# Kernel optimization log

Hardware: AMD Instinct MI355X
Metric: run time of the kernel (lower is better)

## Reference

```python
import jax, jax.numpy as jnp
import numpy as np

B, T, LAGS, H, F = 4096, 256, 32, 128, 2


def setup_inputs() -> dict:
    key = jax.random.key(0)
    ks = jax.random.split(key, 6)
    s = lambda n: 1.0 / np.sqrt(n)
    return {
        "inputs": jax.random.normal(ks[0], (B, T, F), jnp.float32),
        "Wx": jax.random.normal(ks[1], (F, H), jnp.float32) * s(F),
        "Wh": jax.random.normal(ks[2], (H, H), jnp.float32) * s(H),
        "b": jnp.zeros((H,), jnp.float32),
        "Wd": jax.random.normal(ks[3], (H, 1), jnp.float32) * s(H),
        "bd": jnp.zeros((1,), jnp.float32),
        "alpha": jax.random.uniform(ks[4], (1, 1), jnp.float32),
        "lags": LAGS,
    }


def reference(inputs, Wx, Wh, b, Wd, bd, alpha, lags):
    # alpha constrained to [0, 1] (MinMax constraint / clamp in call)
    a = jnp.clip(alpha, 0.0, 1.0)  # [1,1]
    Bsz = inputs.shape[0]
    h0 = jnp.zeros((Bsz, Wh.shape[0]), inputs.dtype)

    def cell(h, x):
        # SimpleRNN cell: tanh(x Wx + h Wh + b)
        return jnp.tanh(x @ Wx + h @ Wh + b)

    # ---- warmup: run RNN over first `lags` steps of the full 2-feature input
    warm_xs = jnp.transpose(inputs[:, :lags], (1, 0, 2))  # [lags, B, F]

    def warm_step(h, x):
        return cell(h, x), None

    h, _ = jax.lax.scan(warm_step, h0, warm_xs)
    pred = h @ Wd + bd  # [B, 1] first prediction (appended un-smoothed)

    # step n consumes exogenous inputs[:, lags + n - 1, 0]
    exog = jnp.transpose(inputs[:, lags:-1, 0])  # [T-lags-1, B]

    def ar_step(carry, e):
        h, pred, es = carry
        x = jnp.concatenate([e[:, None], pred], axis=-1)  # [B, 2]
        h = cell(h, x)
        pred = h @ Wd + bd
        es = a * pred + (1.0 - a) * es  # exponential smoothing blend
        return (h, pred, es), es

    _, es_seq = jax.lax.scan(ar_step, (h, pred, pred), exog)  # [T-lags-1, B, 1]

    preds = jnp.concatenate([pred[None], es_seq], axis=0)  # [T-lags, B, 1]
    return jnp.transpose(preds, (1, 0, 2))  # [B, T-lags, 1]
```

## Files before the change

kernel.cpp:

```cpp
#include <hip/hip_runtime.h>

namespace {

constexpr int kB = 4096;
constexpr int kT = 256;
constexpr int kLags = 32;
constexpr int kH = 128;
constexpr int kSteps = 255;
constexpr int kOut = 224;
constexpr int kMT = 16;
constexpr int kThreads = 256;
constexpr int kHS = 136;
constexpr int kOS = 225;
constexpr int kHLO = 2 * kMT * kHS;

constexpr float kZS = 2.8853900817779268f;

typedef __attribute__((ext_vector_type(8))) short short8;
typedef __attribute__((ext_vector_type(4))) float f32x4;

struct __align__(16) SMem {
    unsigned short hhi[2][kMT][kHS];
    unsigned short hlo[2][kMT][kHS];
    float x0T[kT][kMT];
    float x1wT[kLags][kMT];
    float pbuf[2][4][kMT];
    float obuf[kMT][kOS];
};

__device__ __forceinline__ unsigned short bf16_rne(float f) {
    unsigned u = __builtin_bit_cast(unsigned, f);
    u += 0x7FFFu + ((u >> 16) & 1u);
    return (unsigned short)(u >> 16);
}
__device__ __forceinline__ float bf16_f32(unsigned short h) {
    unsigned u = ((unsigned)h) << 16;
    return __builtin_bit_cast(float, u);
}
__device__ __forceinline__ float tanh_from_zs(float zs) {
    float e = __builtin_amdgcn_exp2f(zs);
    return fmaf(-2.0f, __builtin_amdgcn_rcpf(e + 1.0f), 1.0f);
}
__device__ __forceinline__ unsigned bf16_rne_hibits(float f) {
    unsigned u = __builtin_bit_cast(unsigned, f);
    return (u + (0x7FFFu + ((u >> 16) & 1u))) & 0xFFFF0000u;
}

__global__ __launch_bounds__(kThreads, 1)
void arx_rnn_es_kernel(const float* __restrict__ inputs,
                       const float* __restrict__ Wx,
                       const float* __restrict__ Wh,
                       const float* __restrict__ bias,
                       const float* __restrict__ Wd,
                       const float* __restrict__ bd,
                       const float* __restrict__ alpha,
                       float* __restrict__ out) {
    __shared__ SMem sm;
    const int tid  = threadIdx.x;
    const int b0   = blockIdx.x * kMT;
    const int lane = tid & 63;
    const int w    = tid >> 6;
    const int n    = lane & 15;
    const int q    = lane >> 4;

    for (int idx = tid; idx < kMT * kT; idx += kThreads) {
        const int mm = idx >> 8;
        const int t  = idx & 255;
        float2 v = ((const float2*)inputs)[(size_t)(b0 + mm) * kT + t];
        sm.x0T[t][mm] = v.x;
        if (t < kLags) sm.x1wT[t][mm] = v.y;
    }
    for (int idx = tid; idx < kMT * kHS; idx += kThreads) {
        ((unsigned short*)sm.hhi[0])[idx] = 0;
        ((unsigned short*)sm.hlo[0])[idx] = 0;
    }

    const float av  = fminf(fmaxf(alpha[0], 0.0f), 1.0f);
    const float bdv = bd[0];

    f32x4 sb2v[2], swx0v[2], swx1ev[2], sbpv[2];
#pragma unroll
    for (int t = 0; t < 2; ++t) {
#pragma unroll
        for (int r = 0; r < 4; ++r) {
            const int colE = w * 32 + t * 16 + q * 4 + r;
            const float bc = bias[colE];
            const float w0 = Wx[colE];
            const float w1 = Wx[kH + colE];
            sb2v[t][r]   = kZS * bc;
            swx0v[t][r]  = kZS * w0;
            swx1ev[t][r] = kZS * w1;
            sbpv[t][r]   = kZS * (bc + bdv * w1);
        }
    }
    __syncthreads();

    const f32x4 zero4 = {0.0f, 0.0f, 0.0f, 0.0f};
    int p = 0;

    {
        short8 whh[2][4], whl[2][4];
#pragma unroll
        for (int t = 0; t < 2; ++t) {
            const int colw = w * 32 + t * 16 + n;
#pragma unroll
            for (int c = 0; c < 4; ++c) {
#pragma unroll
                for (int j = 0; j < 8; ++j) {
                    const int k = c * 32 + q * 8 + j;
                    float wv = kZS * Wh[(size_t)k * kH + colw];
                    unsigned short hi = bf16_rne(wv);
                    whh[t][c][j] = (short)hi;
                    whl[t][c][j] = (short)bf16_rne(wv - bf16_f32(hi));
                }
            }
        }

#pragma unroll 1
        for (int st = 0; st < kLags; ++st) {
            const float x0s = sm.x0T[st][n];
            const float x1s = sm.x1wT[st][n];

            const unsigned short* hb = (const unsigned short*)&sm.hhi[p][n][0];
            unsigned short* hw = (unsigned short*)&sm.hhi[p ^ 1][n][0];

            short8 bh[4], bl[4];
#pragma unroll
            for (int c = 0; c < 4; ++c) {
                bh[c] = *(const short8*)(hb + c * 32 + 8 * q);
                bl[c] = *(const short8*)(hb + kHLO + c * 32 + 8 * q);
            }

            f32x4 a1[2], a2[2], a3[2];
#pragma unroll
            for (int t = 0; t < 2; ++t) {
                f32x4 xi;
#pragma unroll
                for (int r = 0; r < 4; ++r)
                    xi[r] = fmaf(x0s, swx0v[t][r], x1s * swx1ev[t][r]);
                a1[t] = __builtin_amdgcn_mfma_f32_16x16x32_bf16(whh[t][0], bh[0], sb2v[t], 0, 0, 0);
                a2[t] = __builtin_amdgcn_mfma_f32_16x16x32_bf16(whl[t][0], bh[0], zero4,   0, 0, 0);
                a3[t] = __builtin_amdgcn_mfma_f32_16x16x32_bf16(whh[t][0], bl[0], xi,      0, 0, 0);
#pragma unroll
                for (int c = 1; c < 4; ++c) {
                    a1[t] = __builtin_amdgcn_mfma_f32_16x16x32_bf16(whh[t][c], bh[c], a1[t], 0, 0, 0);
                    a2[t] = __builtin_amdgcn_mfma_f32_16x16x32_bf16(whl[t][c], bh[c], a2[t], 0, 0, 0);
                    a3[t] = __builtin_amdgcn_mfma_f32_16x16x32_bf16(whh[t][c], bl[c], a3[t], 0, 0, 0);
                }
            }

#pragma unroll
            for (int t = 0; t < 2; ++t) {
                unsigned rb[4], db[4];
#pragma unroll
                for (int r = 0; r < 4; ++r) {
                    float zs = (a1[t][r] + a2[t][r]) + a3[t][r];
                    float hf = tanh_from_zs(zs);
                    rb[r] = bf16_rne_hibits(hf);
                    float d = hf - __builtin_bit_cast(float, rb[r]);
                    db[r] = __builtin_bit_cast(unsigned, d);
                }
                uint2 uh, ul;
                uh.x = __builtin_amdgcn_perm(rb[1], rb[0], 0x07060302u);
                uh.y = __builtin_amdgcn_perm(rb[3], rb[2], 0x07060302u);
                ul.x = __builtin_amdgcn_perm(db[1], db[0], 0x07060302u);
                ul.y = __builtin_amdgcn_perm(db[3], db[2], 0x07060302u);
                *(uint2*)(hw + w * 32 + t * 16 + q * 4) = uh;
                *(uint2*)(hw + kHLO + w * 32 + t * 16 + q * 4) = ul;
            }

            __syncthreads();
            p ^= 1;
        }
    }

    short8 fhh[2][4], fhl[2][4], dhw;
    {
#pragma unroll
        for (int t = 0; t < 2; ++t) {
            const int colw = w * 32 + t * 16 + n;
            const float wx1w = Wx[kH + colw];
#pragma unroll
            for (int c = 0; c < 4; ++c) {
#pragma unroll
                for (int j = 0; j < 8; ++j) {
                    const int k = c * 32 + q * 8 + j;
                    float wv = kZS * fmaf(Wd[k], wx1w, Wh[(size_t)k * kH + colw]);
                    unsigned short hi = bf16_rne(wv);
                    fhh[t][c][j] = (short)hi;
                    fhl[t][c][j] = (short)bf16_rne(wv - bf16_f32(hi));
                }
            }
        }
#pragma unroll
        for (int j = 0; j < 8; ++j)
            dhw[j] = (short)bf16_rne(Wd[w * 32 + q * 8 + j]);
    }

    float es = 0.0f;

#pragma unroll 1
    for (int st = kLags; st < kSteps; ++st) {
        const float x0s = sm.x0T[st][n];

        const unsigned short* hb = (const unsigned short*)&sm.hhi[p][n][0];
        unsigned short* hw = (unsigned short*)&sm.hhi[p ^ 1][n][0];

        short8 bh[4], bl[4];
#pragma unroll
        for (int c = 0; c < 4; ++c) {
            bh[c] = *(const short8*)(hb + c * 32 + 8 * q);
            bl[c] = *(const short8*)(hb + kHLO + c * 32 + 8 * q);
        }
        short8 bhP = *(const short8*)(hb + w * 32 + 8 * q);

        f32x4 a1[2], a2[2], a3[2];
#pragma unroll
        for (int t = 0; t < 2; ++t) {
            f32x4 xi;
#pragma unroll
            for (int r = 0; r < 4; ++r) xi[r] = x0s * swx0v[t][r];
            a1[t] = __builtin_amdgcn_mfma_f32_16x16x32_bf16(fhh[t][0], bh[0], sbpv[t], 0, 0, 0);
            a2[t] = __builtin_amdgcn_mfma_f32_16x16x32_bf16(fhl[t][0], bh[0], zero4,   0, 0, 0);
            a3[t] = __builtin_amdgcn_mfma_f32_16x16x32_bf16(fhh[t][0], bl[0], xi,      0, 0, 0);
#pragma unroll
            for (int c = 1; c < 4; ++c) {
                a1[t] = __builtin_amdgcn_mfma_f32_16x16x32_bf16(fhh[t][c], bh[c], a1[t], 0, 0, 0);
                a2[t] = __builtin_amdgcn_mfma_f32_16x16x32_bf16(fhl[t][c], bh[c], a2[t], 0, 0, 0);
                a3[t] = __builtin_amdgcn_mfma_f32_16x16x32_bf16(fhh[t][c], bl[c], a3[t], 0, 0, 0);
            }
        }

        f32x4 P = __builtin_amdgcn_mfma_f32_16x16x32_bf16(dhw, bhP, zero4, 0, 0, 0);
        if (q == 0) sm.pbuf[p][w][n] = P[0];

        if (w == 0 && q == 0 && st > kLags) {
            float pv = ((sm.pbuf[p ^ 1][0][n] + sm.pbuf[p ^ 1][1][n]) +
                        (sm.pbuf[p ^ 1][2][n] + sm.pbuf[p ^ 1][3][n])) + bdv;
            const int m = st - kLags - 1;
            es = (m == 0) ? pv : fmaf(av, pv - es, es);
            sm.obuf[n][m] = es;
        }

#pragma unroll
        for (int t = 0; t < 2; ++t) {
            unsigned rb[4], db[4];
#pragma unroll
            for (int r = 0; r < 4; ++r) {
                float zs = (a1[t][r] + a2[t][r]) + a3[t][r];
                float hf = tanh_from_zs(zs);
                rb[r] = bf16_rne_hibits(hf);
                float d = hf - __builtin_bit_cast(float, rb[r]);
                db[r] = __builtin_bit_cast(unsigned, d);
            }
            uint2 uh, ul;
            uh.x = __builtin_amdgcn_perm(rb[1], rb[0], 0x07060302u);
            uh.y = __builtin_amdgcn_perm(rb[3], rb[2], 0x07060302u);
            ul.x = __builtin_amdgcn_perm(db[1], db[0], 0x07060302u);
            ul.y = __builtin_amdgcn_perm(db[3], db[2], 0x07060302u);
            *(uint2*)(hw + w * 32 + t * 16 + q * 4) = uh;
            *(uint2*)(hw + kHLO + w * 32 + t * 16 + q * 4) = ul;
        }

        __syncthreads();
        p ^= 1;
    }

    if (w == 0 && q == 0) {
        float pv = ((sm.pbuf[p ^ 1][0][n] + sm.pbuf[p ^ 1][1][n]) +
                    (sm.pbuf[p ^ 1][2][n] + sm.pbuf[p ^ 1][3][n])) + bdv;
        es = fmaf(av, pv - es, es);
        sm.obuf[n][kOut - 2] = es;
    }
    {
        const unsigned short* hb = (const unsigned short*)&sm.hhi[p][n][0];
        short8 bhP = *(const short8*)(hb + w * 32 + 8 * q);
        f32x4 P = __builtin_amdgcn_mfma_f32_16x16x32_bf16(dhw, bhP, zero4, 0, 0, 0);
        if (q == 0) sm.pbuf[p][w][n] = P[0];
    }
    __syncthreads();
    if (w == 0 && q == 0) {
        float pv = ((sm.pbuf[p][0][n] + sm.pbuf[p][1][n]) +
                    (sm.pbuf[p][2][n] + sm.pbuf[p][3][n])) + bdv;
        es = fmaf(av, pv - es, es);
        sm.obuf[n][kOut - 1] = es;
    }

    __syncthreads();
    for (int idx = tid; idx < kMT * kOut; idx += kThreads) {
        const int mm = idx / kOut;
        const int t  = idx - mm * kOut;
        out[(size_t)(b0 + mm) * kOut + t] = sm.obuf[mm][t];
    }
}

}

extern "C" void kernel_launch(void* const* d_in, const int* in_sizes, int n_in,
                              void* d_out, int out_size, void* d_ws, size_t ws_size,
                              hipStream_t stream) {
    const float* inputs = (const float*)d_in[0];
    const float* Wx     = (const float*)d_in[1];
    const float* Wh     = (const float*)d_in[2];
    const float* bias   = (const float*)d_in[3];
    const float* Wd     = (const float*)d_in[4];
    const float* bd     = (const float*)d_in[5];
    const float* alpha  = (const float*)d_in[6];

    arx_rnn_es_kernel<<<kB / kMT, kThreads, 0, stream>>>(
        inputs, Wx, Wh, bias, Wd, bd, alpha, (float*)d_out);
}
```

Baseline: 252.4 us.

## Split hidden columns across eight waves instead of four per block

Doubles the block to 512 threads so each of eight waves owns a 16-column tile of the hidden state rather than two 16-column tiles per wave. Each recurrent step then has a shorter serial MFMA chain per wave and more waves to hide latency. The prediction dot product stays on the first four waves. In exchange every step's barrier now spans twice as many waves, and launch bounds request two blocks per CU, which may not be reachable given the LDS footprint.

Result: faster. 216.6 us (-14.2%).

```diff
diff --git a/kernel.cpp b/kernel.cpp
--- a/kernel.cpp
+++ b/kernel.cpp
@@ -9,7 +9,7 @@
 constexpr int kSteps = 255;
 constexpr int kOut = 224;
 constexpr int kMT = 16;
-constexpr int kThreads = 256;
+constexpr int kThreads = 512;
 constexpr int kHS = 136;
 constexpr int kOS = 225;
 constexpr int kHLO = 2 * kMT * kHS;
@@ -46,7 +46,7 @@
     return (u + (0x7FFFu + ((u >> 16) & 1u))) & 0xFFFF0000u;
 }
 
-__global__ __launch_bounds__(kThreads, 1)
+__global__ __launch_bounds__(kThreads, 2)
 void arx_rnn_es_kernel(const float* __restrict__ inputs,
                        const float* __restrict__ Wx,
                        const float* __restrict__ Wh,
@@ -78,20 +78,17 @@
     const float av  = fminf(fmaxf(alpha[0], 0.0f), 1.0f);
     const float bdv = bd[0];
 
-    f32x4 sb2v[2], swx0v[2], swx1ev[2], sbpv[2];
-#pragma unroll
-    for (int t = 0; t < 2; ++t) {
-#pragma unroll
-        for (int r = 0; r < 4; ++r) {
-            const int colE = w * 32 + t * 16 + q * 4 + r;
-            const float bc = bias[colE];
-            const float w0 = Wx[colE];
-            const float w1 = Wx[kH + colE];
-            sb2v[t][r]   = kZS * bc;
-            swx0v[t][r]  = kZS * w0;
-            swx1ev[t][r] = kZS * w1;
-            sbpv[t][r]   = kZS * (bc + bdv * w1);
-        }
+    f32x4 sb2v, swx0v, swx1ev, sbpv;
+#pragma unroll
+    for (int r = 0; r < 4; ++r) {
+        const int colE = w * 16 + q * 4 + r;
+        const float bc = bias[colE];
+        const float w0 = Wx[colE];
+        const float w1 = Wx[kH + colE];
+        sb2v[r]   = kZS * bc;
+        swx0v[r]  = kZS * w0;
+        swx1ev[r] = kZS * w1;
+        sbpv[r]   = kZS * (bc + bdv * w1);
     }
     __syncthreads();
 
@@ -99,10 +96,9 @@
     int p = 0;
 
     {
-        short8 whh[2][4], whl[2][4];
-#pragma unroll
-        for (int t = 0; t < 2; ++t) {
-            const int colw = w * 32 + t * 16 + n;
+        short8 whh[4], whl[4];
+        {
+            const int colw = w * 16 + n;
 #pragma unroll
             for (int c = 0; c < 4; ++c) {
 #pragma unroll
@@ -110,8 +106,8 @@
                     const int k = c * 32 + q * 8 + j;
                     float wv = kZS * Wh[(size_t)k * kH + colw];
                     unsigned short hi = bf16_rne(wv);
-                    whh[t][c][j] = (short)hi;
-                    whl[t][c][j] = (short)bf16_rne(wv - bf16_f32(hi));
+                    whh[c][j] = (short)hi;
+                    whl[c][j] = (short)bf16_rne(wv - bf16_f32(hi));
                 }
             }
         }
@@ -131,70 +127,66 @@
                 bl[c] = *(const short8*)(hb + kHLO + c * 32 + 8 * q);
             }
 
-            f32x4 a1[2], a2[2], a3[2];
-#pragma unroll
-            for (int t = 0; t < 2; ++t) {
-                f32x4 xi;
-#pragma unroll
-                for (int r = 0; r < 4; ++r)
-                    xi[r] = fmaf(x0s, swx0v[t][r], x1s * swx1ev[t][r]);
-                a1[t] = __builtin_amdgcn_mfma_f32_16x16x32_bf16(whh[t][0], bh[0], sb2v[t], 0, 0, 0);
-                a2[t] = __builtin_amdgcn_mfma_f32_16x16x32_bf16(whl[t][0], bh[0], zero4,   0, 0, 0);
-                a3[t] = __builtin_amdgcn_mfma_f32_16x16x32_bf16(whh[t][0], bl[0], xi,      0, 0, 0);
-#pragma unroll
-                for (int c = 1; c < 4; ++c) {
-                    a1[t] = __builtin_amdgcn_mfma_f32_16x16x32_bf16(whh[t][c], bh[c], a1[t], 0, 0, 0);
-                    a2[t] = __builtin_amdgcn_mfma_f32_16x16x32_bf16(whl[t][c], bh[c], a2[t], 0, 0, 0);
-                    a3[t] = __builtin_amdgcn_mfma_f32_16x16x32_bf16(whh[t][c], bl[c], a3[t], 0, 0, 0);
-                }
-            }
-
-#pragma unroll
-            for (int t = 0; t < 2; ++t) {
-                unsigned rb[4], db[4];
-#pragma unroll
-                for (int r = 0; r < 4; ++r) {
-                    float zs = (a1[t][r] + a2[t][r]) + a3[t][r];
-                    float hf = tanh_from_zs(zs);
-                    rb[r] = bf16_rne_hibits(hf);
-                    float d = hf - __builtin_bit_cast(float, rb[r]);
-                    db[r] = __builtin_bit_cast(unsigned, d);
-                }
-                uint2 uh, ul;
-                uh.x = __builtin_amdgcn_perm(rb[1], rb[0], 0x07060302u);
-                uh.y = __builtin_amdgcn_perm(rb[3], rb[2], 0x07060302u);
-                ul.x = __builtin_amdgcn_perm(db[1], db[0], 0x07060302u);
-                ul.y = __builtin_amdgcn_perm(db[3], db[2], 0x07060302u);
-                *(uint2*)(hw + w * 32 + t * 16 + q * 4) = uh;
-                *(uint2*)(hw + kHLO + w * 32 + t * 16 + q * 4) = ul;
-            }
+            f32x4 xi;
+#pragma unroll
+            for (int r = 0; r < 4; ++r)
+                xi[r] = fmaf(x0s, swx0v[r], x1s * swx1ev[r]);
+
+            f32x4 a1 = __builtin_amdgcn_mfma_f32_16x16x32_bf16(whh[0], bh[0], sb2v, 0, 0, 0);
+            f32x4 a2 = __builtin_amdgcn_mfma_f32_16x16x32_bf16(whl[0], bh[0], zero4, 0, 0, 0);
+            f32x4 a3 = __builtin_amdgcn_mfma_f32_16x16x32_bf16(whh[0], bl[0], xi,   0, 0, 0);
+#pragma unroll
+            for (int c = 1; c < 4; ++c) {
+                a1 = __builtin_amdgcn_mfma_f32_16x16x32_bf16(whh[c], bh[c], a1, 0, 0, 0);
+                a2 = __builtin_amdgcn_mfma_f32_16x16x32_bf16(whl[c], bh[c], a2, 0, 0, 0);
+                a3 = __builtin_amdgcn_mfma_f32_16x16x32_bf16(whh[c], bl[c], a3, 0, 0, 0);
+            }
+
+            unsigned rb[4], db[4];
+#pragma unroll
+            for (int r = 0; r < 4; ++r) {
+                float zs = (a1[r] + a2[r]) + a3[r];
+                float hf = tanh_from_zs(zs);
+                rb[r] = bf16_rne_hibits(hf);
+                float d = hf - __builtin_bit_cast(float, rb[r]);
+                db[r] = __builtin_bit_cast(unsigned, d);
+            }
+            uint2 uh, ul;
+            uh.x = __builtin_amdgcn_perm(rb[1], rb[0], 0x07060302u);
+            uh.y = __builtin_amdgcn_perm(rb[3], rb[2], 0x07060302u);
+            ul.x = __builtin_amdgcn_perm(db[1], db[0], 0x07060302u);
+            ul.y = __builtin_amdgcn_perm(db[3], db[2], 0x07060302u);
+            const int wcol = w * 16 + q * 4;
+            *(uint2*)(hw + wcol) = uh;
+            *(uint2*)(hw + kHLO + wcol) = ul;
 
             __syncthreads();
             p ^= 1;
         }
     }
 
-    short8 fhh[2][4], fhl[2][4], dhw;
+    short8 fhh[4], fhl[4], dhw;
     {
-#pragma unroll
-        for (int t = 0; t < 2; ++t) {
-            const int colw = w * 32 + t * 16 + n;
-            const float wx1w = Wx[kH + colw];
-#pragma unroll
-            for (int c = 0; c < 4; ++c) {
-#pragma unroll
-                for (int j = 0; j < 8; ++j) {
-                    const int k = c * 32 + q * 8 + j;
-                    float wv = kZS * fmaf(Wd[k], wx1w, Wh[(size_t)k * kH + colw]);
-                    unsigned short hi = bf16_rne(wv);
-                    fhh[t][c][j] = (short)hi;
-                    fhl[t][c][j] = (short)bf16_rne(wv - bf16_f32(hi));
-                }
-            }
-        }
-#pragma unroll
-        for (int j = 0; j < 8; ++j)
-            dhw[j] = (short)bf16_rne(Wd[w * 32 + q * 8 + j]);
+        const int colw = w * 16 + n;
+        const float wx1w = Wx[kH + colw];
+#pragma unroll
+        for (int c = 0; c < 4; ++c) {
+#pragma unroll
+            for (int j = 0; j < 8; ++j) {
+                const int k = c * 32 + q * 8 + j;
+                float wv = kZS * fmaf(Wd[k], wx1w, Wh[(size_t)k * kH + colw]);
+                unsigned short hi = bf16_rne(wv);
+                fhh[c][j] = (short)hi;
+                fhl[c][j] = (short)bf16_rne(wv - bf16_f32(hi));
+            }
+        }
+        if (w < 4) {
+#pragma unroll
+            for (int j = 0; j < 8; ++j)
+                dhw[j] = (short)bf16_rne(Wd[w * 32 + q * 8 + j]);
+        } else {
+            dhw = short8{0, 0, 0, 0, 0, 0, 0, 0};
+        }
     }
 
     float es = 0.0f;
@@ -205,34 +197,6 @@
 
         const unsigned short* hb = (const unsigned short*)&sm.hhi[p][n][0];
         unsigned short* hw = (unsigned short*)&sm.hhi[p ^ 1][n][0];
-
-        short8 bh[4], bl[4];
-#pragma unroll
-        for (int c = 0; c < 4; ++c) {
-            bh[c] = *(const short8*)(hb + c * 32 + 8 * q);
-            bl[c] = *(const short8*)(hb + kHLO + c * 32 + 8 * q);
-        }
-        short8 bhP = *(const short8*)(hb + w * 32 + 8 * q);
-
-        f32x4 a1[2], a2[2], a3[2];
-#pragma unroll
-        for (int t = 0; t < 2; ++t) {
-            f32x4 xi;
-#pragma unroll
-            for (int r = 0; r < 4; ++r) xi[r] = x0s * swx0v[t][r];
-            a1[t] = __builtin_amdgcn_mfma_f32_16x16x32_bf16(fhh[t][0], bh[0], sbpv[t], 0, 0, 0);
-            a2[t] = __builtin_amdgcn_mfma_f32_16x16x32_bf16(fhl[t][0], bh[0], zero4,   0, 0, 0);
-            a3[t] = __builtin_amdgcn_mfma_f32_16x16x32_bf16(fhh[t][0], bl[0], xi,      0, 0, 0);
-#pragma unroll
-            for (int c = 1; c < 4; ++c) {
-                a1[t] = __builtin_amdgcn_mfma_f32_16x16x32_bf16(fhh[t][c], bh[c], a1[t], 0, 0, 0);
-                a2[t] = __builtin_amdgcn_mfma_f32_16x16x32_bf16(fhl[t][c], bh[c], a2[t], 0, 0, 0);
-                a3[t] = __builtin_amdgcn_mfma_f32_16x16x32_bf16(fhh[t][c], bl[c], a3[t], 0, 0, 0);
-            }
-        }
-
-        f32x4 P = __builtin_amdgcn_mfma_f32_16x16x32_bf16(dhw, bhP, zero4, 0, 0, 0);
-        if (q == 0) sm.pbuf[p][w][n] = P[0];
 
         if (w == 0 && q == 0 && st > kLags) {
             float pv = ((sm.pbuf[p ^ 1][0][n] + sm.pbuf[p ^ 1][1][n]) +
@@ -242,25 +206,50 @@
             sm.obuf[n][m] = es;
         }
 
-#pragma unroll
-        for (int t = 0; t < 2; ++t) {
-            unsigned rb[4], db[4];
-#pragma unroll
-            for (int r = 0; r < 4; ++r) {
-                float zs = (a1[t][r] + a2[t][r]) + a3[t][r];
-                float hf = tanh_from_zs(zs);
-                rb[r] = bf16_rne_hibits(hf);
-                float d = hf - __builtin_bit_cast(float, rb[r]);
-                db[r] = __builtin_bit_cast(unsigned, d);
-            }
-            uint2 uh, ul;
-            uh.x = __builtin_amdgcn_perm(rb[1], rb[0], 0x07060302u);
-            uh.y = __builtin_amdgcn_perm(rb[3], rb[2], 0x07060302u);
-            ul.x = __builtin_amdgcn_perm(db[1], db[0], 0x07060302u);
-            ul.y = __builtin_amdgcn_perm(db[3], db[2], 0x07060302u);
-            *(uint2*)(hw + w * 32 + t * 16 + q * 4) = uh;
-            *(uint2*)(hw + kHLO + w * 32 + t * 16 + q * 4) = ul;
-        }
+        short8 bh[4], bl[4];
+#pragma unroll
+        for (int c = 0; c < 4; ++c) {
+            bh[c] = *(const short8*)(hb + c * 32 + 8 * q);
+            bl[c] = *(const short8*)(hb + kHLO + c * 32 + 8 * q);
+        }
+
+        f32x4 xi;
+#pragma unroll
+        for (int r = 0; r < 4; ++r) xi[r] = x0s * swx0v[r];
+
+        f32x4 a1 = __builtin_amdgcn_mfma_f32_16x16x32_bf16(fhh[0], bh[0], sbpv, 0, 0, 0);
+        f32x4 a2 = __builtin_amdgcn_mfma_f32_16x16x32_bf16(fhl[0], bh[0], zero4, 0, 0, 0);
+        f32x4 a3 = __builtin_amdgcn_mfma_f32_16x16x32_bf16(fhh[0], bl[0], xi,   0, 0, 0);
+#pragma unroll
+        for (int c = 1; c < 4; ++c) {
+            a1 = __builtin_amdgcn_mfma_f32_16x16x32_bf16(fhh[c], bh[c], a1, 0, 0, 0);
+            a2 = __builtin_amdgcn_mfma_f32_16x16x32_bf16(fhl[c], bh[c], a2, 0, 0, 0);
+            a3 = __builtin_amdgcn_mfma_f32_16x16x32_bf16(fhh[c], bl[c], a3, 0, 0, 0);
+        }
+
+        if (w < 4) {
+            short8 bhP = *(const short8*)(hb + w * 32 + 8 * q);
+            f32x4 P = __builtin_amdgcn_mfma_f32_16x16x32_bf16(dhw, bhP, zero4, 0, 0, 0);
+            if (q == 0) sm.pbuf[p][w][n] = P[0];
+        }
+
+        unsigned rb[4], db[4];
+#pragma unroll
+        for (int r = 0; r < 4; ++r) {
+            float zs = (a1[r] + a2[r]) + a3[r];
+            float hf = tanh_from_zs(zs);
+            rb[r] = bf16_rne_hibits(hf);
+            float d = hf - __builtin_bit_cast(float, rb[r]);
+            db[r] = __builtin_bit_cast(unsigned, d);
+        }
+        uint2 uh, ul;
+        uh.x = __builtin_amdgcn_perm(rb[1], rb[0], 0x07060302u);
+        uh.y = __builtin_amdgcn_perm(rb[3], rb[2], 0x07060302u);
+        ul.x = __builtin_amdgcn_perm(db[1], db[0], 0x07060302u);
+        ul.y = __builtin_amdgcn_perm(db[3], db[2], 0x07060302u);
+        const int wcol = w * 16 + q * 4;
+        *(uint2*)(hw + wcol) = uh;
+        *(uint2*)(hw + kHLO + wcol) = ul;
 
         __syncthreads();
         p ^= 1;
@@ -272,7 +261,7 @@
         es = fmaf(av, pv - es, es);
         sm.obuf[n][kOut - 2] = es;
     }
-    {
+    if (w < 4) {
         const unsigned short* hb = (const unsigned short*)&sm.hhi[p][n][0];
         short8 bhP = *(const short8*)(hb + w * 32 + 8 * q);
         f32x4 P = __builtin_amdgcn_mfma_f32_16x16x32_bf16(dhw, bhP, zero4, 0, 0, 0);
```

## Split recurrent matmul across two warp groups with shared-memory handoff

Applied to the files above, without the earlier changes.

Doubles the block to 8 waves. Waves 0-3 compute the hi/lo weight products against the hi part of the hidden state, plus tanh. Waves 4-7 compute the correction product against the low part of the hidden state and pass it through a bf16 shared buffer. The prediction dot product and the exponential smoothing also move to the second group, so that work overlaps with the tanh phase. This shortens each wave's serial MFMA chain per step. In exchange it adds a second __syncthreads per step and rounds the correction term to bf16.

New measurement: 282.3 us. 1.12x slower.

```diff
diff --git a/kernel.cpp b/kernel.cpp
--- a/kernel.cpp
+++ b/kernel.cpp
@@ -9,10 +9,11 @@
 constexpr int kSteps = 255;
 constexpr int kOut = 224;
 constexpr int kMT = 16;
-constexpr int kThreads = 256;
+constexpr int kThreads = 512;
 constexpr int kHS = 136;
 constexpr int kOS = 225;
 constexpr int kHLO = 2 * kMT * kHS;
+constexpr int kAS = 20;
 
 constexpr float kZS = 2.8853900817779268f;
 
@@ -24,6 +25,7 @@
     unsigned short hlo[2][kMT][kHS];
     float x0T[kT][kMT];
     float x1wT[kLags][kMT];
+    unsigned short abuf[8][kMT][kAS];
     float pbuf[2][4][kMT];
     float obuf[kMT][kOS];
 };
@@ -46,7 +48,7 @@
     return (u + (0x7FFFu + ((u >> 16) & 1u))) & 0xFFFF0000u;
 }
 
-__global__ __launch_bounds__(kThreads, 1)
+__global__ __launch_bounds__(kThreads, 2)
 void arx_rnn_es_kernel(const float* __restrict__ inputs,
                        const float* __restrict__ Wx,
                        const float* __restrict__ Wh,
@@ -60,15 +62,17 @@
     const int b0   = blockIdx.x * kMT;
     const int lane = tid & 63;
     const int w    = tid >> 6;
+    const int v    = w & 3;
+    const bool hrole = (w < 4);
     const int n    = lane & 15;
     const int q    = lane >> 4;
 
     for (int idx = tid; idx < kMT * kT; idx += kThreads) {
         const int mm = idx >> 8;
         const int t  = idx & 255;
-        float2 v = ((const float2*)inputs)[(size_t)(b0 + mm) * kT + t];
-        sm.x0T[t][mm] = v.x;
-        if (t < kLags) sm.x1wT[t][mm] = v.y;
+        float2 val = ((const float2*)inputs)[(size_t)(b0 + mm) * kT + t];
+        sm.x0T[t][mm] = val.x;
+        if (t < kLags) sm.x1wT[t][mm] = val.y;
     }
     for (int idx = tid; idx < kMT * kHS; idx += kThreads) {
         ((unsigned short*)sm.hhi[0])[idx] = 0;
@@ -79,18 +83,20 @@
     const float bdv = bd[0];
 
     f32x4 sb2v[2], swx0v[2], swx1ev[2], sbpv[2];
-#pragma unroll
-    for (int t = 0; t < 2; ++t) {
-#pragma unroll
-        for (int r = 0; r < 4; ++r) {
-            const int colE = w * 32 + t * 16 + q * 4 + r;
-            const float bc = bias[colE];
-            const float w0 = Wx[colE];
-            const float w1 = Wx[kH + colE];
-            sb2v[t][r]   = kZS * bc;
-            swx0v[t][r]  = kZS * w0;
-            swx1ev[t][r] = kZS * w1;
-            sbpv[t][r]   = kZS * (bc + bdv * w1);
+    if (hrole) {
+#pragma unroll
+        for (int t = 0; t < 2; ++t) {
+#pragma unroll
+            for (int r = 0; r < 4; ++r) {
+                const int colE = v * 32 + t * 16 + q * 4 + r;
+                const float bc = bias[colE];
+                const float w0 = Wx[colE];
+                const float w1 = Wx[kH + colE];
+                sb2v[t][r]   = kZS * bc;
+                swx0v[t][r]  = kZS * w0;
+                swx1ev[t][r] = kZS * w1;
+                sbpv[t][r]   = kZS * (bc + bdv * w1);
+            }
         }
     }
     __syncthreads();
@@ -99,10 +105,10 @@
     int p = 0;
 
     {
-        short8 whh[2][4], whl[2][4];
+        short8 wHi[2][4], wLo[2][4];
 #pragma unroll
         for (int t = 0; t < 2; ++t) {
-            const int colw = w * 32 + t * 16 + n;
+            const int colw = v * 32 + t * 16 + n;
 #pragma unroll
             for (int c = 0; c < 4; ++c) {
 #pragma unroll
@@ -110,51 +116,183 @@
                     const int k = c * 32 + q * 8 + j;
                     float wv = kZS * Wh[(size_t)k * kH + colw];
                     unsigned short hi = bf16_rne(wv);
-                    whh[t][c][j] = (short)hi;
-                    whl[t][c][j] = (short)bf16_rne(wv - bf16_f32(hi));
+                    wHi[t][c][j] = (short)hi;
+                    if (hrole) wLo[t][c][j] = (short)bf16_rne(wv - bf16_f32(hi));
                 }
             }
         }
 
 #pragma unroll 1
         for (int st = 0; st < kLags; ++st) {
+            f32x4 A1[2], A2[2], A3[2];
+            if (hrole) {
+                const float x0s = sm.x0T[st][n];
+                const float x1s = sm.x1wT[st][n];
+                const unsigned short* hb = (const unsigned short*)&sm.hhi[p][n][0];
+                short8 bh[4];
+#pragma unroll
+                for (int c = 0; c < 4; ++c)
+                    bh[c] = *(const short8*)(hb + c * 32 + 8 * q);
+#pragma unroll
+                for (int t = 0; t < 2; ++t) {
+                    f32x4 xi;
+#pragma unroll
+                    for (int r = 0; r < 4; ++r)
+                        xi[r] = fmaf(x0s, swx0v[t][r], x1s * swx1ev[t][r]);
+                    A1[t] = __builtin_amdgcn_mfma_f32_16x16x32_bf16(wHi[t][0], bh[0], sb2v[t], 0, 0, 0);
+                    A2[t] = __builtin_amdgcn_mfma_f32_16x16x32_bf16(wLo[t][0], bh[0], xi,      0, 0, 0);
+#pragma unroll
+                    for (int c = 1; c < 4; ++c) {
+                        A1[t] = __builtin_amdgcn_mfma_f32_16x16x32_bf16(wHi[t][c], bh[c], A1[t], 0, 0, 0);
+                        A2[t] = __builtin_amdgcn_mfma_f32_16x16x32_bf16(wLo[t][c], bh[c], A2[t], 0, 0, 0);
+                    }
+                }
+            } else {
+                const unsigned short* hb = (const unsigned short*)&sm.hhi[p][n][0];
+                short8 bl[4];
+#pragma unroll
+                for (int c = 0; c < 4; ++c)
+                    bl[c] = *(const short8*)(hb + kHLO + c * 32 + 8 * q);
+#pragma unroll
+                for (int t = 0; t < 2; ++t) {
+                    A3[t] = __builtin_amdgcn_mfma_f32_16x16x32_bf16(wHi[t][0], bl[0], zero4, 0, 0, 0);
+#pragma unroll
+                    for (int c = 1; c < 4; ++c)
+                        A3[t] = __builtin_amdgcn_mfma_f32_16x16x32_bf16(wHi[t][c], bl[c], A3[t], 0, 0, 0);
+                    unsigned rb0 = bf16_rne_hibits(A3[t][0]);
+                    unsigned rb1 = bf16_rne_hibits(A3[t][1]);
+                    unsigned rb2 = bf16_rne_hibits(A3[t][2]);
+                    unsigned rb3 = bf16_rne_hibits(A3[t][3]);
+                    uint2 ua;
+                    ua.x = __builtin_amdgcn_perm(rb1, rb0, 0x07060302u);
+                    ua.y = __builtin_amdgcn_perm(rb3, rb2, 0x07060302u);
+                    *(uint2*)&sm.abuf[2 * v + t][n][4 * q] = ua;
+                }
+            }
+            __syncthreads();
+
+            if (hrole) {
+                unsigned short* hw = (unsigned short*)&sm.hhi[p ^ 1][n][0];
+#pragma unroll
+                for (int t = 0; t < 2; ++t) {
+                    uint2 a3p = *(const uint2*)&sm.abuf[2 * v + t][n][4 * q];
+                    float a3f[4];
+                    a3f[0] = __builtin_bit_cast(float, a3p.x << 16);
+                    a3f[1] = __builtin_bit_cast(float, a3p.x & 0xFFFF0000u);
+                    a3f[2] = __builtin_bit_cast(float, a3p.y << 16);
+                    a3f[3] = __builtin_bit_cast(float, a3p.y & 0xFFFF0000u);
+                    unsigned rb[4], db[4];
+#pragma unroll
+                    for (int r = 0; r < 4; ++r) {
+                        float zs = (A1[t][r] + A2[t][r]) + a3f[r];
+                        float hf = tanh_from_zs(zs);
+                        rb[r] = bf16_rne_hibits(hf);
+                        float d = hf - __builtin_bit_cast(float, rb[r]);
+                        db[r] = __builtin_bit_cast(unsigned, d);
+                    }
+                    uint2 uh, ul;
+                    uh.x = __builtin_amdgcn_perm(rb[1], rb[0], 0x07060302u);
+                    uh.y = __builtin_amdgcn_perm(rb[3], rb[2], 0x07060302u);
+                    ul.x = __builtin_amdgcn_perm(db[1], db[0], 0x07060302u);
+                    ul.y = __builtin_amdgcn_perm(db[3], db[2], 0x07060302u);
+                    const int wcol = v * 32 + t * 16 + q * 4;
+                    *(uint2*)(hw + wcol) = uh;
+                    *(uint2*)(hw + kHLO + wcol) = ul;
+                }
+            }
+            __syncthreads();
+            p ^= 1;
+        }
+    }
+
+    short8 fHi[2][4], fLo[2][4], dhv;
+    {
+#pragma unroll
+        for (int t = 0; t < 2; ++t) {
+            const int colw = v * 32 + t * 16 + n;
+            const float wx1w = Wx[kH + colw];
+#pragma unroll
+            for (int c = 0; c < 4; ++c) {
+#pragma unroll
+                for (int j = 0; j < 8; ++j) {
+                    const int k = c * 32 + q * 8 + j;
+                    float wv = kZS * fmaf(Wd[k], wx1w, Wh[(size_t)k * kH + colw]);
+                    unsigned short hi = bf16_rne(wv);
+                    fHi[t][c][j] = (short)hi;
+                    if (hrole) fLo[t][c][j] = (short)bf16_rne(wv - bf16_f32(hi));
+                }
+            }
+        }
+        if (!hrole) {
+#pragma unroll
+            for (int j = 0; j < 8; ++j)
+                dhv[j] = (short)bf16_rne(Wd[v * 32 + q * 8 + j]);
+        }
+    }
+
+    float es = 0.0f;
+
+#pragma unroll 1
+    for (int st = kLags; st < kSteps; ++st) {
+        f32x4 A1[2], A2[2];
+        if (hrole) {
             const float x0s = sm.x0T[st][n];
-            const float x1s = sm.x1wT[st][n];
-
             const unsigned short* hb = (const unsigned short*)&sm.hhi[p][n][0];
-            unsigned short* hw = (unsigned short*)&sm.hhi[p ^ 1][n][0];
-
-            short8 bh[4], bl[4];
-#pragma unroll
-            for (int c = 0; c < 4; ++c) {
+            short8 bh[4];
+#pragma unroll
+            for (int c = 0; c < 4; ++c)
                 bh[c] = *(const short8*)(hb + c * 32 + 8 * q);
-                bl[c] = *(const short8*)(hb + kHLO + c * 32 + 8 * q);
-            }
-
-            f32x4 a1[2], a2[2], a3[2];
 #pragma unroll
             for (int t = 0; t < 2; ++t) {
                 f32x4 xi;
 #pragma unroll
-                for (int r = 0; r < 4; ++r)
-                    xi[r] = fmaf(x0s, swx0v[t][r], x1s * swx1ev[t][r]);
-                a1[t] = __builtin_amdgcn_mfma_f32_16x16x32_bf16(whh[t][0], bh[0], sb2v[t], 0, 0, 0);
-                a2[t] = __builtin_amdgcn_mfma_f32_16x16x32_bf16(whl[t][0], bh[0], zero4,   0, 0, 0);
-                a3[t] = __builtin_amdgcn_mfma_f32_16x16x32_bf16(whh[t][0], bl[0], xi,      0, 0, 0);
+                for (int r = 0; r < 4; ++r) xi[r] = x0s * swx0v[t][r];
+                A1[t] = __builtin_amdgcn_mfma_f32_16x16x32_bf16(fHi[t][0], bh[0], sbpv[t], 0, 0, 0);
+                A2[t] = __builtin_amdgcn_mfma_f32_16x16x32_bf16(fLo[t][0], bh[0], xi,      0, 0, 0);
 #pragma unroll
                 for (int c = 1; c < 4; ++c) {
-                    a1[t] = __builtin_amdgcn_mfma_f32_16x16x32_bf16(whh[t][c], bh[c], a1[t], 0, 0, 0);
-                    a2[t] = __builtin_amdgcn_mfma_f32_16x16x32_bf16(whl[t][c], bh[c], a2[t], 0, 0, 0);
-                    a3[t] = __builtin_amdgcn_mfma_f32_16x16x32_bf16(whh[t][c], bl[c], a3[t], 0, 0, 0);
-                }
-            }
-
+                    A1[t] = __builtin_amdgcn_mfma_f32_16x16x32_bf16(fHi[t][c], bh[c], A1[t], 0, 0, 0);
+                    A2[t] = __builtin_amdgcn_mfma_f32_16x16x32_bf16(fLo[t][c], bh[c], A2[t], 0, 0, 0);
+                }
+            }
+        } else {
+            const unsigned short* hb = (const unsigned short*)&sm.hhi[p][n][0];
+            short8 bl[4];
+#pragma unroll
+            for (int c = 0; c < 4; ++c)
+                bl[c] = *(const short8*)(hb + kHLO + c * 32 + 8 * q);
 #pragma unroll
             for (int t = 0; t < 2; ++t) {
+                f32x4 A3 = __builtin_amdgcn_mfma_f32_16x16x32_bf16(fHi[t][0], bl[0], zero4, 0, 0, 0);
+#pragma unroll
+                for (int c = 1; c < 4; ++c)
+                    A3 = __builtin_amdgcn_mfma_f32_16x16x32_bf16(fHi[t][c], bl[c], A3, 0, 0, 0);
+                unsigned rb0 = bf16_rne_hibits(A3[0]);
+                unsigned rb1 = bf16_rne_hibits(A3[1]);
+                unsigned rb2 = bf16_rne_hibits(A3[2]);
+                unsigned rb3 = bf16_rne_hibits(A3[3]);
+                uint2 ua;
+                ua.x = __builtin_amdgcn_perm(rb1, rb0, 0x07060302u);
+                ua.y = __builtin_amdgcn_perm(rb3, rb2, 0x07060302u);
+                *(uint2*)&sm.abuf[2 * v + t][n][4 * q] = ua;
+            }
+        }
+        __syncthreads();
+
+        if (hrole) {
+            unsigned short* hw = (unsigned short*)&sm.hhi[p ^ 1][n][0];
+#pragma unroll
+            for (int t = 0; t < 2; ++t) {
+                uint2 a3p = *(const uint2*)&sm.abuf[2 * v + t][n][4 * q];
+                float a3f[4];
+                a3f[0] = __builtin_bit_cast(float, a3p.x << 16);
+                a3f[1] = __builtin_bit_cast(float, a3p.x & 0xFFFF0000u);
+                a3f[2] = __builtin_bit_cast(float, a3p.y << 16);
+                a3f[3] = __builtin_bit_cast(float, a3p.y & 0xFFFF0000u);
                 unsigned rb[4], db[4];
 #pragma unroll
                 for (int r = 0; r < 4; ++r) {
-                    float zs = (a1[t][r] + a2[t][r]) + a3[t][r];
+                    float zs = (A1[t][r] + A2[t][r]) + a3f[r];
                     float hf = tanh_from_zs(zs);
                     rb[r] = bf16_rne_hibits(hf);
                     float d = hf - __builtin_bit_cast(float, rb[r]);
@@ -165,121 +303,42 @@
                 uh.y = __builtin_amdgcn_perm(rb[3], rb[2], 0x07060302u);
                 ul.x = __builtin_amdgcn_perm(db[1], db[0], 0x07060302u);
                 ul.y = __builtin_amdgcn_perm(db[3], db[2], 0x07060302u);
-                *(uint2*)(hw + w * 32 + t * 16 + q * 4) = uh;
-                *(uint2*)(hw + kHLO + w * 32 + t * 16 + q * 4) = ul;
-            }
-
-            __syncthreads();
-            p ^= 1;
-        }
-    }
-
-    short8 fhh[2][4], fhl[2][4], dhw;
-    {
-#pragma unroll
-        for (int t = 0; t < 2; ++t) {
-            const int colw = w * 32 + t * 16 + n;
-            const float wx1w = Wx[kH + colw];
-#pragma unroll
-            for (int c = 0; c < 4; ++c) {
-#pragma unroll
-                for (int j = 0; j < 8; ++j) {
-                    const int k = c * 32 + q * 8 + j;
-                    float wv = kZS * fmaf(Wd[k], wx1w, Wh[(size_t)k * kH + colw]);
-                    unsigned short hi = bf16_rne(wv);
-                    fhh[t][c][j] = (short)hi;
-                    fhl[t][c][j] = (short)bf16_rne(wv - bf16_f32(hi));
-                }
-            }
-        }
-#pragma unroll
-        for (int j = 0; j < 8; ++j)
-            dhw[j] = (short)bf16_rne(Wd[w * 32 + q * 8 + j]);
-    }
-
-    float es = 0.0f;
-
-#pragma unroll 1
-    for (int st = kLags; st < kSteps; ++st) {
-        const float x0s = sm.x0T[st][n];
-
-        const unsigned short* hb = (const unsigned short*)&sm.hhi[p][n][0];
-        unsigned short* hw = (unsigned short*)&sm.hhi[p ^ 1][n][0];
-
-        short8 bh[4], bl[4];
-#pragma unroll
-        for (int c = 0; c < 4; ++c) {
-            bh[c] = *(const short8*)(hb + c * 32 + 8 * q);
-            bl[c] = *(const short8*)(hb + kHLO + c * 32 + 8 * q);
-        }
-        short8 bhP = *(const short8*)(hb + w * 32 + 8 * q);
-
-        f32x4 a1[2], a2[2], a3[2];
-#pragma unroll
-        for (int t = 0; t < 2; ++t) {
-            f32x4 xi;
-#pragma unroll
-            for (int r = 0; r < 4; ++r) xi[r] = x0s * swx0v[t][r];
-            a1[t] = __builtin_amdgcn_mfma_f32_16x16x32_bf16(fhh[t][0], bh[0], sbpv[t], 0, 0, 0);
-            a2[t] = __builtin_amdgcn_mfma_f32_16x16x32_bf16(fhl[t][0], bh[0], zero4,   0, 0, 0);
-            a3[t] = __builtin_amdgcn_mfma_f32_16x16x32_bf16(fhh[t][0], bl[0], xi,      0, 0, 0);
-#pragma unroll
-            for (int c = 1; c < 4; ++c) {
-                a1[t] = __builtin_amdgcn_mfma_f32_16x16x32_bf16(fhh[t][c], bh[c], a1[t], 0, 0, 0);
-                a2[t] = __builtin_amdgcn_mfma_f32_16x16x32_bf16(fhl[t][c], bh[c], a2[t], 0, 0, 0);
-                a3[t] = __builtin_amdgcn_mfma_f32_16x16x32_bf16(fhh[t][c], bl[c], a3[t], 0, 0, 0);
-            }
-        }
-
-        f32x4 P = __builtin_amdgcn_mfma_f32_16x16x32_bf16(dhw, bhP, zero4, 0, 0, 0);
-        if (q == 0) sm.pbuf[p][w][n] = P[0];
-
-        if (w == 0 && q == 0 && st > kLags) {
-            float pv = ((sm.pbuf[p ^ 1][0][n] + sm.pbuf[p ^ 1][1][n]) +
-                        (sm.pbuf[p ^ 1][2][n] + sm.pbuf[p ^ 1][3][n])) + bdv;
-            const int m = st - kLags - 1;
-            es = (m == 0) ? pv : fmaf(av, pv - es, es);
-            sm.obuf[n][m] = es;
-        }
-
-#pragma unroll
-        for (int t = 0; t < 2; ++t) {
-            unsigned rb[4], db[4];
-#pragma unroll
-            for (int r = 0; r < 4; ++r) {
-                float zs = (a1[t][r] + a2[t][r]) + a3[t][r];
-                float hf = tanh_from_zs(zs);
-                rb[r] = bf16_rne_hibits(hf);
-                float d = hf - __builtin_bit_cast(float, rb[r]);
-                db[r] = __builtin_bit_cast(unsigned, d);
-            }
-            uint2 uh, ul;
-            uh.x = __builtin_amdgcn_perm(rb[1], rb[0], 0x07060302u);
-            uh.y = __builtin_amdgcn_perm(rb[3], rb[2], 0x07060302u);
-            ul.x = __builtin_amdgcn_perm(db[1], db[0], 0x07060302u);
-            ul.y = __builtin_amdgcn_perm(db[3], db[2], 0x07060302u);
-            *(uint2*)(hw + w * 32 + t * 16 + q * 4) = uh;
-            *(uint2*)(hw + kHLO + w * 32 + t * 16 + q * 4) = ul;
-        }
-
+                const int wcol = v * 32 + t * 16 + q * 4;
+                *(uint2*)(hw + wcol) = uh;
+                *(uint2*)(hw + kHLO + wcol) = ul;
+            }
+        } else {
+            const unsigned short* hb = (const unsigned short*)&sm.hhi[p][n][0];
+            short8 bhP = *(const short8*)(hb + v * 32 + 8 * q);
+            f32x4 P = __builtin_amdgcn_mfma_f32_16x16x32_bf16(dhv, bhP, zero4, 0, 0, 0);
+            if (q == 0) sm.pbuf[p][v][n] = P[0];
+
+            if (w == 4 && q == 0 && st > kLags) {
+                float pv = ((sm.pbuf[p ^ 1][0][n] + sm.pbuf[p ^ 1][1][n]) +
+                            (sm.pbuf[p ^ 1][2][n] + sm.pbuf[p ^ 1][3][n])) + bdv;
+                const int m = st - kLags - 1;
+                es = (m == 0) ? pv : fmaf(av, pv - es, es);
+                sm.obuf[n][m] = es;
+            }
+        }
         __syncthreads();
         p ^= 1;
     }
 
-    if (w == 0 && q == 0) {
+    if (w == 4 && q == 0) {
         float pv = ((sm.pbuf[p ^ 1][0][n] + sm.pbuf[p ^ 1][1][n]) +
                     (sm.pbuf[p ^ 1][2][n] + sm.pbuf[p ^ 1][3][n])) + bdv;
         es = fmaf(av, pv - es, es);
         sm.obuf[n][kOut - 2] = es;
     }
-    {
+    if (!hrole) {
         const unsigned short* hb = (const unsigned short*)&sm.hhi[p][n][0];
-        short8 bhP = *(const short8*)(hb + w * 32 + 8 * q);
-        f32x4 P = __builtin_amdgcn_mfma_f32_16x16x32_bf16(dhw, bhP, zero4, 0, 0, 0);
-        if (q == 0) sm.pbuf[p][w][n] = P[0];
+        short8 bhP = *(const short8*)(hb + v * 32 + 8 * q);
+        f32x4 P = __builtin_amdgcn_mfma_f32_16x16x32_bf16(dhv, bhP, zero4, 0, 0, 0);
+        if (q == 0) sm.pbuf[p][v][n] = P[0];
     }
     __syncthreads();
-    if (w == 0 && q == 0) {
+    if (w == 4 && q == 0) {
         float pv = ((sm.pbuf[p][0][n] + sm.pbuf[p][1][n]) +
                     (sm.pbuf[p][2][n] + sm.pbuf[p][3][n])) + bdv;
         es = fmaf(av, pv - es, es);
```
